# Performance work log

Measured on AMD Instinct MI355X. Metric: run time of the kernel, lower is better.

## Reference

```python
import jax, jax.numpy as jnp
import numpy as np
from jax import lax

K = 8
SCALE = 100.0

# ---- straight-through binarizers (match torch custom Functions) ----
@jax.custom_vjp
def bin_w(x):
    return jnp.sign(x)

def _bin_w_fwd(x):
    return jnp.sign(x), None

def _bin_w_bwd(_, g):
    return (g,)  # identity STE

bin_w.defvjp(_bin_w_fwd, _bin_w_bwd)

@jax.custom_vjp
def bin_a(x):
    return jnp.sign(x)

def _bin_a_fwd(x):
    return jnp.sign(x), x

def _bin_a_bwd(x, g):
    return (g * jnp.clip(2.0 - jnp.abs(2.0 * x), 0.0, None),)

bin_a.defvjp(_bin_a_fwd, _bin_a_bwd)

# ---- SDP sampling with custom backward (grad_z scaled by sqrt(scale)) ----
@jax.custom_vjp
def sdp(m, z, rv):
    # m: (N,), z: (K,N), rv: (1,K) -> w: (N,)
    return (rv @ z)[0] + m

def _sdp_fwd(m, z, rv):
    return (rv @ z)[0] + m, rv

def _sdp_bwd(rv, g):
    grad_m = g
    grad_z = (rv.T @ g[None, :]) * np.sqrt(SCALE)  # (K,N)
    return (grad_m, grad_z, jnp.zeros_like(rv))

sdp.defvjp(_sdp_fwd, _sdp_bwd)

def _forward(x, M, Z, alpha, rv):
    N = M.size
    m = M.reshape(N)          # (N,)
    z = Z.reshape(K, N)       # (K,N)
    # no_grad normalization of m,z data: value changes, gradient passes through identity
    A = m * m + jnp.sum(z * z, axis=0) / SCALE
    inv = lax.rsqrt(A)
    m_used = m + lax.stop_gradient(m * inv - m)
    z_used = z + lax.stop_gradient(z * inv - z)
    w = sdp(m_used, z_used, rv)               # (N,)
    bw = bin_w(w).reshape(M.shape)            # (O,I,3,3) in {-1,+1}
    ba = bin_a(x)                             # (B,C,H,W) in {-1,+1}
    out = lax.conv_general_dilated(
        ba, bw, window_strides=(1, 1), padding=((1, 1), (1, 1)),
        dimension_numbers=('NCHW', 'OIHW', 'NCHW'))
    return out * alpha  # alpha (O,1,1) broadcasts over (B,O,H,W)

def setup_inputs() -> dict:
    key = jax.random.key(0)
    k1, k2, k3, k4, k5 = jax.random.split(key, 5)
    x = jax.random.normal(k1, (64, 256, 28, 28), dtype=jnp.float32)
    M = jax.random.normal(k2, (256, 256, 3, 3), dtype=jnp.float32)
    Z = jax.random.normal(k3, (8, 256, 256, 3, 3), dtype=jnp.float32)
    alpha = jax.random.uniform(k4, (256, 1, 1), dtype=jnp.float32)
    rv = jax.random.normal(k5, (1, 8), dtype=jnp.float32) * np.float32(1.0 / np.sqrt(SCALE))
    return {"x": x, "M": M, "Z": Z, "alpha": alpha, "rv": rv}

def reference(x, M, Z, alpha, rv):
    return _forward(x, M, Z, alpha, rv)
```

## Files before the change

kernel.cpp:

```cpp
#include <hip/hip_runtime.h>
#include <stdint.h>

typedef unsigned int uint32;

#define BB 64
#define CC 256
#define OO 256
#define HH 28
#define WW 28
#define HWP 784
#define NWT 589824

__global__ __launch_bounds__(256) void pack_x_kernel(
    const float* __restrict__ x, uint32* __restrict__ apack) {
  int p = blockIdx.x * 256 + threadIdx.x;
  int j = blockIdx.y;
  int b = blockIdx.z;
  if (p >= HWP) return;
  const float* xp = x + ((size_t)(b * CC + j * 32) * HWP) + p;
  uint32 m = 0;
#pragma unroll
  for (int cc = 0; cc < 32; ++cc) {
    float v = xp[(size_t)cc * HWP];
    m |= ((uint32)(v > 0.0f)) << cc;
  }
  apack[((size_t)b * HWP + p) * 8 + j] = m;
}

__global__ __launch_bounds__(256) void pack_w_kernel(
    const float* __restrict__ M, const float* __restrict__ Z,
    const float* __restrict__ rv, const float* __restrict__ alpha,
    uint32* __restrict__ wpack, float* __restrict__ ptabA,
    uint32* __restrict__ ptabP) {
  __shared__ float sacc[2304];
  __shared__ uint32 ww[72];
  const int o = blockIdx.x;
  const int tid = threadIdx.x;
  const size_t base = (size_t)o * 2304;

  float r[8];
#pragma unroll
  for (int k = 0; k < 8; ++k) r[k] = rv[k];

#pragma unroll
  for (int ii = 0; ii < 9; ++ii) {
    int i = tid + ii * 256;
    float s = M[base + i];
#pragma unroll
    for (int k = 0; k < 8; ++k) s += r[k] * Z[(size_t)k * NWT + base + i];
    sacc[i] = s;
  }
  __syncthreads();

  if (tid < 72) {
    int tap = tid % 9;
    int j = tid / 9;
    uint32 m = 0;
#pragma unroll
    for (int cc = 0; cc < 32; ++cc) {
      float v = sacc[(j * 32 + cc) * 9 + tap];
      m |= ((uint32)(v > 0.0f)) << cc;
    }
    ww[tap * 8 + j] = m;
    wpack[(size_t)o * 72 + tap * 8 + j] = m;
  }
  __syncthreads();

  if (tid == 0) {
    int pt[9];
#pragma unroll
    for (int t = 0; t < 9; ++t) {
      int s = 0;
#pragma unroll
      for (int j = 0; j < 8; ++j) s += __popc(ww[t * 8 + j]);
      pt[t] = s;
    }
    int row0 = pt[0] + pt[1] + pt[2], row2 = pt[6] + pt[7] + pt[8];
    int col0 = pt[0] + pt[3] + pt[6], col2 = pt[2] + pt[5] + pt[8];
    float a = alpha[o];
    const int nv[9] = {4, 6, 4, 6, 9, 6, 4, 6, 4};
    int S[9];
    S[0] = row0 + col0 - pt[0]; S[1] = row0; S[2] = row0 + col2 - pt[2];
    S[3] = col0;                S[4] = 0;    S[5] = col2;
    S[6] = row2 + col0 - pt[6]; S[7] = row2; S[8] = row2 + col2 - pt[8];
#pragma unroll
    for (int c = 0; c < 9; ++c)
      ptabA[o * 9 + c] = a * (float)(256 * nv[c] + 2 * S[c]);
    ptabP[o * 4 + 0] = __float_as_uint(-2.0f * a);
    ptabP[o * 4 + 1] = (uint32)col0;
    ptabP[o * 4 + 2] = (uint32)col2;
    ptabP[o * 4 + 3] = 0;
  }
}

#define BCNT_ACC(T, x) asm("v_bcnt_u32_b32 %0, %1, %0" : "+v"(T) : "v"(x))

__global__ __launch_bounds__(256, 4) void conv_kernel(
    const uint32* __restrict__ apack, const uint32* __restrict__ wpack,
    const float* __restrict__ ptabA, const uint32* __restrict__ ptabP,
    float* __restrict__ out) {
  __shared__ float atab[16 * 9];

  const int rg = blockIdx.x;
  const int og = blockIdx.y;
  const int b  = blockIdx.z;
  const int tid = threadIdx.x;
  const int lane = tid & 63;
  const int wv = tid >> 6;
  const int w = lane & 31;
  const int rb = rg * 16 + wv * 4 + (lane >> 5) * 2;
  const bool wact = w < WW;

  if (tid < 144) atab[tid] = ptabA[og * 144 + tid];
  __syncthreads();

  const int wcl = wact ? w : (WW - 1);
  uint4 A[4][2];
#pragma unroll
  for (int i = 0; i < 4; ++i) {
    int rr = rb - 1 + i;
    bool v = (rr >= 0) && (rr < HH);
    const uint4* src =
        (const uint4*)(apack + ((size_t)(b * HWP + (v ? rr : 0) * WW + wcl)) * 8);
    uint4 lo = src[0], hi = src[1];
    if (!v) { lo = make_uint4(0, 0, 0, 0); hi = make_uint4(0, 0, 0, 0); }
    A[i][0] = lo;
    A[i][1] = hi;
  }
  {
    uint32* aw = (uint32*)A;
#pragma unroll
    for (int i = 0; i < 32; i += 4)
      asm volatile("" : "+v"(aw[i]), "+v"(aw[i + 1]), "+v"(aw[i + 2]),
                        "+v"(aw[i + 3]));
  }

  const int wc = (w == 0) ? 0 : (w == WW - 1 ? 2 : 1);
  const int r1v = rb + 1;
  const int hc0 = (rb == 0) ? 0 : (rb == HH - 1 ? 2 : 1);
  const int hc1 = (r1v == 0) ? 0 : (r1v == HH - 1 ? 2 : 1);
  const int cls0 = hc0 * 3 + wc;
  const int cls1 = hc1 * 3 + wc;

  const size_t obase = ((size_t)b * OO + og * 16) * HWP + (size_t)rb * WW + w;
  const bool st0 = wact && (rb < HH);
  const bool st1 = wact && (r1v < HH);

  for (int oi = 0; oi < 16; ++oi) {
    const int o = og * 16 + oi;
    const int wo = __builtin_amdgcn_readfirstlane(o * 72);
    const uint32* wt = wpack + wo;
    const uint4 pm = ((const uint4*)ptabP)[o];
    const float m = __uint_as_float(pm.x);

    uint32 T00 = 0, T01 = 0, T02 = 0, T10 = 0, T11 = 0, T12 = 0;
#pragma unroll
    for (int dh = 0; dh < 3; ++dh) {
      const uint32* a0 = (const uint32*)&A[dh][0];
      const uint32* a1 = (const uint32*)&A[dh + 1][0];
#pragma unroll
      for (int j = 0; j < 8; ++j) {
        const uint32 w0 = wt[(dh * 3 + 0) * 8 + j];
        const uint32 w1 = wt[(dh * 3 + 1) * 8 + j];
        const uint32 w2 = wt[(dh * 3 + 2) * 8 + j];
        const uint32 av0 = a0[j], av1 = a1[j];
        BCNT_ACC(T00, av0 ^ w0);
        BCNT_ACC(T01, av0 ^ w1);
        BCNT_ACC(T02, av0 ^ w2);
        BCNT_ACC(T10, av1 ^ w0);
        BCNT_ACC(T11, av1 ^ w1);
        BCNT_ACC(T12, av1 ^ w2);
      }
    }
    uint32 pl = __shfl_up(T00 | (T10 << 16), 1);
    uint32 pr = __shfl_down(T02 | (T12 << 16), 1);
    if (w == 0)      pl = pm.y * 0x10001u;
    if (w == WW - 1) pr = pm.z * 0x10001u;
    uint32 tp = pl + (T01 | (T11 << 16)) + pr;
    float r0 = fmaf(m, (float)(tp & 0xffffu), atab[oi * 9 + cls0]);
    float r1 = fmaf(m, (float)(tp >> 16), atab[oi * 9 + cls1]);
    if (st0) out[obase + (size_t)oi * HWP] = r0;
    if (st1) out[obase + (size_t)oi * HWP + WW] = r1;
  }
}

extern "C" void kernel_launch(void* const* d_in, const int* in_sizes, int n_in,
                              void* d_out, int out_size, void* d_ws,
                              size_t ws_size, hipStream_t stream) {
  const float* x     = (const float*)d_in[0];
  const float* M     = (const float*)d_in[1];
  const float* Z     = (const float*)d_in[2];
  const float* alpha = (const float*)d_in[3];
  const float* rv    = (const float*)d_in[4];
  float* out = (float*)d_out;

  uint32* apack = (uint32*)d_ws;
  uint32* wpack = (uint32*)((char*)d_ws + 1605632);
  float*  ptabA = (float*)((char*)d_ws + 1679360);
  uint32* ptabP = (uint32*)((char*)d_ws + 1688576);

  pack_x_kernel<<<dim3(4, 8, BB), 256, 0, stream>>>(x, apack);
  pack_w_kernel<<<dim3(256), 256, 0, stream>>>(M, Z, rv, alpha, wpack, ptabA,
                                               ptabP);
  conv_kernel<<<dim3(2, 16, BB), 256, 0, stream>>>(apack, wpack, ptabA, ptabP,
                                                   out);
}
```

Before: 187.6 us.

## Replace XNOR-popcount binary conv with int8 MFMA implicit GEMM on padded input

```diff
diff --git a/kernel.cpp b/kernel.cpp
--- a/kernel.cpp
+++ b/kernel.cpp
@@ -2,6 +2,8 @@
 #include <stdint.h>
 
 typedef unsigned int uint32;
+typedef unsigned char u8;
+typedef int v4i __attribute__((ext_vector_type(4)));
 
 #define BB 64
 #define CC 256
@@ -10,38 +12,48 @@
 #define WW 28
 #define HWP 784
 #define NWT 589824
+#define HP 30
+#define XBSTR (HP * HP * 256)
+#define WTAP (256 * 256)
 
-__global__ __launch_bounds__(256) void pack_x_kernel(
-    const float* __restrict__ x, uint32* __restrict__ apack) {
-  int p = blockIdx.x * 256 + threadIdx.x;
-  int j = blockIdx.y;
-  int b = blockIdx.z;
-  if (p >= HWP) return;
-  const float* xp = x + ((size_t)(b * CC + j * 32) * HWP) + p;
-  uint32 m = 0;
+__global__ __launch_bounds__(256) void cast_x_kernel(
+    const float* __restrict__ x, u8* __restrict__ xi8) {
+  const int hp = blockIdx.x;
+  const int b  = blockIdx.y;
+  const int tid = threadIdx.x;
+  const int wp = tid & 31;
+  const int cq0 = tid >> 5;
+  if (wp >= HP) return;
+  u8* row = xi8 + (size_t)b * XBSTR + (size_t)(hp * HP + wp) * 256;
+  const bool interior = (hp >= 1) && (hp <= 28) && (wp >= 1) && (wp <= 28);
+  const float* xp =
+      x + (((size_t)b * 256) * 28 + (hp - 1)) * 28 + (wp - 1);
 #pragma unroll
-  for (int cc = 0; cc < 32; ++cc) {
-    float v = xp[(size_t)cc * HWP];
-    m |= ((uint32)(v > 0.0f)) << cc;
+  for (int it = 0; it < 8; ++it) {
+    const int cq = it * 8 + cq0;
+    uint32 v = 0;
+    if (interior) {
+      const float* p = xp + (size_t)(cq * 4) * HWP;
+      uint32 b0 = (p[0] > 0.f) ? 0x01u : 0xFFu;
+      uint32 b1 = (p[HWP] > 0.f) ? 0x01u : 0xFFu;
+      uint32 b2 = (p[2 * HWP] > 0.f) ? 0x01u : 0xFFu;
+      uint32 b3 = (p[3 * HWP] > 0.f) ? 0x01u : 0xFFu;
+      v = b0 | (b1 << 8) | (b2 << 16) | (b3 << 24);
+    }
+    *(uint32*)(row + cq * 4) = v;
   }
-  apack[((size_t)b * HWP + p) * 8 + j] = m;
 }
 
-__global__ __launch_bounds__(256) void pack_w_kernel(
+__global__ __launch_bounds__(256) void cast_w_kernel(
     const float* __restrict__ M, const float* __restrict__ Z,
-    const float* __restrict__ rv, const float* __restrict__ alpha,
-    uint32* __restrict__ wpack, float* __restrict__ ptabA,
-    uint32* __restrict__ ptabP) {
+    const float* __restrict__ rv, u8* __restrict__ wi8) {
   __shared__ float sacc[2304];
-  __shared__ uint32 ww[72];
   const int o = blockIdx.x;
   const int tid = threadIdx.x;
   const size_t base = (size_t)o * 2304;
-
   float r[8];
 #pragma unroll
   for (int k = 0; k < 8; ++k) r[k] = rv[k];
-
 #pragma unroll
   for (int ii = 0; ii < 9; ++ii) {
     int i = tid + ii * 256;
@@ -51,136 +63,83 @@
     sacc[i] = s;
   }
   __syncthreads();
-
-  if (tid < 72) {
-    int tap = tid % 9;
-    int j = tid / 9;
-    uint32 m = 0;
+  const int c = tid;
 #pragma unroll
-    for (int cc = 0; cc < 32; ++cc) {
-      float v = sacc[(j * 32 + cc) * 9 + tap];
-      m |= ((uint32)(v > 0.0f)) << cc;
-    }
-    ww[tap * 8 + j] = m;
-    wpack[(size_t)o * 72 + tap * 8 + j] = m;
-  }
-  __syncthreads();
-
-  if (tid == 0) {
-    int pt[9];
-#pragma unroll
-    for (int t = 0; t < 9; ++t) {
-      int s = 0;
-#pragma unroll
-      for (int j = 0; j < 8; ++j) s += __popc(ww[t * 8 + j]);
-      pt[t] = s;
-    }
-    int row0 = pt[0] + pt[1] + pt[2], row2 = pt[6] + pt[7] + pt[8];
-    int col0 = pt[0] + pt[3] + pt[6], col2 = pt[2] + pt[5] + pt[8];
-    float a = alpha[o];
-    const int nv[9] = {4, 6, 4, 6, 9, 6, 4, 6, 4};
-    int S[9];
-    S[0] = row0 + col0 - pt[0]; S[1] = row0; S[2] = row0 + col2 - pt[2];
-    S[3] = col0;                S[4] = 0;    S[5] = col2;
-    S[6] = row2 + col0 - pt[6]; S[7] = row2; S[8] = row2 + col2 - pt[8];
-#pragma unroll
-    for (int c = 0; c < 9; ++c)
-      ptabA[o * 9 + c] = a * (float)(256 * nv[c] + 2 * S[c]);
-    ptabP[o * 4 + 0] = __float_as_uint(-2.0f * a);
-    ptabP[o * 4 + 1] = (uint32)col0;
-    ptabP[o * 4 + 2] = (uint32)col2;
-    ptabP[o * 4 + 3] = 0;
+  for (int t = 0; t < 9; ++t) {
+    float s = sacc[c * 9 + t];
+    wi8[((size_t)t * 256 + o) * 256 + c] = (s > 0.f) ? (u8)1 : (u8)0xFF;
   }
 }
 
-#define BCNT_ACC(T, x) asm("v_bcnt_u32_b32 %0, %1, %0" : "+v"(T) : "v"(x))
+__global__ __launch_bounds__(64, 2) void conv_mfma_kernel(
+    const u8* __restrict__ xi8, const u8* __restrict__ wi8,
+    const float* __restrict__ alpha, float* __restrict__ out) {
+  const int lane = threadIdx.x;
+  const int l15 = lane & 15;
+  const int lk  = lane >> 4;
+  const int pixb = blockIdx.x * 112;
+  const int wv   = blockIdx.y;
+  const int b    = blockIdx.z;
 
-__global__ __launch_bounds__(256, 4) void conv_kernel(
-    const uint32* __restrict__ apack, const uint32* __restrict__ wpack,
-    const float* __restrict__ ptabA, const uint32* __restrict__ ptabP,
-    float* __restrict__ out) {
-  __shared__ float atab[16 * 9];
+  int aoff[7];
+#pragma unroll
+  for (int mt = 0; mt < 7; ++mt) {
+    int p = pixb + mt * 16 + l15;
+    int h = p / 28, w = p - h * 28;
+    aoff[mt] = (h * HP + w) * 256 + lk * 16;
+  }
+  const u8* Ab = xi8 + (size_t)b * XBSTR;
+  const u8* Bt = wi8 + wv * (64 * 256);
+  const int bvoff = l15 * 256 + lk * 16;
 
-  const int rg = blockIdx.x;
-  const int og = blockIdx.y;
-  const int b  = blockIdx.z;
-  const int tid = threadIdx.x;
-  const int lane = tid & 63;
-  const int wv = tid >> 6;
-  const int w = lane & 31;
-  const int rb = rg * 16 + wv * 4 + (lane >> 5) * 2;
-  const bool wact = w < WW;
+  float aval[4];
+#pragma unroll
+  for (int ot = 0; ot < 4; ++ot) aval[ot] = alpha[wv * 64 + ot * 16 + l15];
 
-  if (tid < 144) atab[tid] = ptabA[og * 144 + tid];
-  __syncthreads();
+  v4i acc[7][4];
+#pragma unroll
+  for (int mt = 0; mt < 7; ++mt)
+#pragma unroll
+    for (int ot = 0; ot < 4; ++ot) acc[mt][ot] = v4i{0, 0, 0, 0};
 
-  const int wcl = wact ? w : (WW - 1);
-  uint4 A[4][2];
+  for (int tap = 0; tap < 9; ++tap) {
 #pragma unroll
-  for (int i = 0; i < 4; ++i) {
-    int rr = rb - 1 + i;
-    bool v = (rr >= 0) && (rr < HH);
-    const uint4* src =
-        (const uint4*)(apack + ((size_t)(b * HWP + (v ? rr : 0) * WW + wcl)) * 8);
-    uint4 lo = src[0], hi = src[1];
-    if (!v) { lo = make_uint4(0, 0, 0, 0); hi = make_uint4(0, 0, 0, 0); }
-    A[i][0] = lo;
-    A[i][1] = hi;
-  }
-  {
-    uint32* aw = (uint32*)A;
+    for (int ks = 0; ks < 4; ++ks) {
+      v4i Bf[4];
 #pragma unroll
-    for (int i = 0; i < 32; i += 4)
-      asm volatile("" : "+v"(aw[i]), "+v"(aw[i + 1]), "+v"(aw[i + 2]),
-                        "+v"(aw[i + 3]));
+      for (int ot = 0; ot < 4; ++ot)
+        Bf[ot] = *(const v4i*)(Bt + (bvoff + ot * 4096 + ks * 64));
+      v4i Af[7];
+#pragma unroll
+      for (int mt = 0; mt < 7; ++mt)
+        Af[mt] = *(const v4i*)(Ab + (aoff[mt] + ks * 64));
+#pragma unroll
+      for (int mt = 0; mt < 7; ++mt)
+#pragma unroll
+        for (int ot = 0; ot < 4; ++ot)
+          acc[mt][ot] = __builtin_amdgcn_mfma_i32_16x16x64_i8(
+              Af[mt], Bf[ot], acc[mt][ot], 0, 0, 0);
+    }
+    const int del = (tap == 2 || tap == 5) ? 7168 : 256;
+#pragma unroll
+    for (int mt = 0; mt < 7; ++mt) aoff[mt] += del;
+    Bt += WTAP;
   }
 
-  const int wc = (w == 0) ? 0 : (w == WW - 1 ? 2 : 1);
-  const int r1v = rb + 1;
-  const int hc0 = (rb == 0) ? 0 : (rb == HH - 1 ? 2 : 1);
-  const int hc1 = (r1v == 0) ? 0 : (r1v == HH - 1 ? 2 : 1);
-  const int cls0 = hc0 * 3 + wc;
-  const int cls1 = hc1 * 3 + wc;
-
-  const size_t obase = ((size_t)b * OO + og * 16) * HWP + (size_t)rb * WW + w;
-  const bool st0 = wact && (rb < HH);
-  const bool st1 = wact && (r1v < HH);
-
-  for (int oi = 0; oi < 16; ++oi) {
-    const int o = og * 16 + oi;
-    const int wo = __builtin_amdgcn_readfirstlane(o * 72);
-    const uint32* wt = wpack + wo;
-    const uint4 pm = ((const uint4*)ptabP)[o];
-    const float m = __uint_as_float(pm.x);
-
-    uint32 T00 = 0, T01 = 0, T02 = 0, T10 = 0, T11 = 0, T12 = 0;
 #pragma unroll
-    for (int dh = 0; dh < 3; ++dh) {
-      const uint32* a0 = (const uint32*)&A[dh][0];
-      const uint32* a1 = (const uint32*)&A[dh + 1][0];
+  for (int mt = 0; mt < 7; ++mt) {
+    const int prow = pixb + mt * 16 + lk * 4;
 #pragma unroll
-      for (int j = 0; j < 8; ++j) {
-        const uint32 w0 = wt[(dh * 3 + 0) * 8 + j];
-        const uint32 w1 = wt[(dh * 3 + 1) * 8 + j];
-        const uint32 w2 = wt[(dh * 3 + 2) * 8 + j];
-        const uint32 av0 = a0[j], av1 = a1[j];
-        BCNT_ACC(T00, av0 ^ w0);
-        BCNT_ACC(T01, av0 ^ w1);
-        BCNT_ACC(T02, av0 ^ w2);
-        BCNT_ACC(T10, av1 ^ w0);
-        BCNT_ACC(T11, av1 ^ w1);
-        BCNT_ACC(T12, av1 ^ w2);
-      }
+    for (int ot = 0; ot < 4; ++ot) {
+      float* op = out +
+          ((size_t)b * 256 + (wv * 64 + ot * 16 + l15)) * HWP + prow;
+      float4 vst;
+      vst.x = aval[ot] * (float)acc[mt][ot][0];
+      vst.y = aval[ot] * (float)acc[mt][ot][1];
+      vst.z = aval[ot] * (float)acc[mt][ot][2];
+      vst.w = aval[ot] * (float)acc[mt][ot][3];
+      *(float4*)op = vst;
     }
-    uint32 pl = __shfl_up(T00 | (T10 << 16), 1);
-    uint32 pr = __shfl_down(T02 | (T12 << 16), 1);
-    if (w == 0)      pl = pm.y * 0x10001u;
-    if (w == WW - 1) pr = pm.z * 0x10001u;
-    uint32 tp = pl + (T01 | (T11 << 16)) + pr;
-    float r0 = fmaf(m, (float)(tp & 0xffffu), atab[oi * 9 + cls0]);
-    float r1 = fmaf(m, (float)(tp >> 16), atab[oi * 9 + cls1]);
-    if (st0) out[obase + (size_t)oi * HWP] = r0;
-    if (st1) out[obase + (size_t)oi * HWP + WW] = r1;
   }
 }
 
@@ -194,14 +153,10 @@
   const float* rv    = (const float*)d_in[4];
   float* out = (float*)d_out;
 
-  uint32* apack = (uint32*)d_ws;
-  uint32* wpack = (uint32*)((char*)d_ws + 1605632);
-  float*  ptabA = (float*)((char*)d_ws + 1679360);
-  uint32* ptabP = (uint32*)((char*)d_ws + 1688576);
+  u8* xi8 = (u8*)d_ws;
+  u8* wi8 = (u8*)d_ws + 14745600;
 
-  pack_x_kernel<<<dim3(4, 8, BB), 256, 0, stream>>>(x, apack);
-  pack_w_kernel<<<dim3(256), 256, 0, stream>>>(M, Z, rv, alpha, wpack, ptabA,
-                                               ptabP);
-  conv_kernel<<<dim3(2, 16, BB), 256, 0, stream>>>(apack, wpack, ptabA, ptabP,
-                                                   out);
+  cast_x_kernel<<<dim3(HP, BB), 256, 0, stream>>>(x, xi8);
+  cast_w_kernel<<<dim3(256), 256, 0, stream>>>(M, Z, rv, wi8);
+  conv_mfma_kernel<<<dim3(7, 4, BB), 64, 0, stream>>>(xi8, wi8, alpha, out);
 }
```

New measurement: 227.1 us. 21.0% more time.
